# Kernel tuning notes

Hardware: AMD Instinct MI355X
Metric: run time of the kernel (lower is better)

## Reference

```python
import jax, jax.numpy as jnp
import numpy as np

B, T, IN = 4096, 512, 1
H, L = 50, 2


def setup_inputs() -> dict:
    key = jax.random.key(0)
    ks = jax.random.split(key, 11)
    s_in = 1.0 / np.sqrt(H)  # PyTorch LSTM init scale
    def u(k, shape):
        return jax.random.uniform(k, shape, jnp.float32, -s_in, s_in)
    return {
        "x": jax.random.normal(ks[0], (B, T, IN), jnp.float32),
        # layer 0 (gate order i, f, g, o stacked along first axis, like torch)
        "W_ih0": u(ks[1], (4 * H, IN)),
        "W_hh0": u(ks[2], (4 * H, H)),
        "b_ih0": u(ks[3], (4 * H,)),
        "b_hh0": u(ks[4], (4 * H,)),
        # layer 1
        "W_ih1": u(ks[5], (4 * H, H)),
        "W_hh1": u(ks[6], (4 * H, H)),
        "b_ih1": u(ks[7], (4 * H,)),
        "b_hh1": u(ks[8], (4 * H,)),
        # final linear projection hidden -> 1
        "fc_w": u(ks[9], (1, H)),
        "fc_b": u(ks[10], (1,)),
    }


def _lstm_layer(x_tbf, W_ih, W_hh, b_ih, b_hh):
    """x_tbf: [T, B, F] -> outputs [T, B, H]. Zero initial (h, c)."""
    # Precompute input contribution for all timesteps at once: [T, B, 4H]
    gates_x = jnp.einsum('tbf,gf->tbg', x_tbf, W_ih) + b_ih + b_hh

    def step(carry, gx):
        h, c = carry
        g = gx + h @ W_hh.T  # [B, 4H]
        i, f, gg, o = jnp.split(g, 4, axis=-1)
        i = jax.nn.sigmoid(i)
        f = jax.nn.sigmoid(f)
        gg = jnp.tanh(gg)
        o = jax.nn.sigmoid(o)
        c = f * c + i * gg
        h = o * jnp.tanh(c)
        return (h, c), h

    Bsz = x_tbf.shape[1]
    h0 = jnp.zeros((Bsz, W_hh.shape[1]), x_tbf.dtype)
    (_, _), hs = jax.lax.scan(step, (h0, h0), gates_x)
    return hs  # [T, B, H]


def reference(x, W_ih0, W_hh0, b_ih0, b_hh0, W_ih1, W_hh1, b_ih1, b_hh1, fc_w, fc_b):
    x_tbf = jnp.transpose(x, (1, 0, 2))  # [T, B, IN]
    h1 = _lstm_layer(x_tbf, W_ih0, W_hh0, b_ih0, b_hh0)   # [T, B, H]
    h2 = _lstm_layer(h1, W_ih1, W_hh1, b_ih1, b_hh1)      # [T, B, H]
    last = h2[-1]                                         # [B, H] == out[:, -1, :]
    return last @ fc_w.T + fc_b                           # [B, 1]
```

## Files before the change

### kernel.cpp

```cpp
#include <hip/hip_runtime.h>


typedef _Float16 half8 __attribute__((ext_vector_type(8)));
typedef float    f32x4 __attribute__((ext_vector_type(4)));

#define TT   512
#define HID  50
#define NB   16

__device__ __forceinline__ float sigm(float v) {
    return __builtin_amdgcn_rcpf(1.0f + __expf(-v));
}
__device__ __forceinline__ float tanhh(float v) {
    return 1.0f - 2.0f * __builtin_amdgcn_rcpf(1.0f + __expf(2.0f * v));
}

__device__ __forceinline__ float4 make_wfrag(const float* W, const float* Wx,
                                             int gate, int cell, int chunk,
                                             int quad, bool foldx) {
    half8 hv = {};
    #pragma unroll
    for (int j = 0; j < 8; ++j) {
        const int k = 32 * chunk + 8 * quad + j;
        float v = 0.0f;
        if (cell < HID) {
            if (k < HID)                 v = W[(gate * HID + cell) * HID + k];
            else if (foldx && k == HID)  v = Wx[gate * HID + cell];
        }
        hv[j] = (_Float16)v;
    }
    return __builtin_bit_cast(float4, hv);
}

#define PIN(f) asm volatile("" : "+v"(f.x), "+v"(f.y), "+v"(f.z), "+v"(f.w));
#define MFMA(af, b, c) __builtin_amdgcn_mfma_f32_16x16x32_f16(__builtin_bit_cast(half8, (af)), (b), (c), 0, 0, 0)

extern "C" __global__ __launch_bounds__(832, 4)
void lstm2_mfma_kernel(const float* __restrict__ x,
                       const float* __restrict__ W_ih0, const float* __restrict__ W_hh0,
                       const float* __restrict__ b_ih0, const float* __restrict__ b_hh0,
                       const float* __restrict__ W_ih1, const float* __restrict__ W_hh1,
                       const float* __restrict__ b_ih1, const float* __restrict__ b_hh1,
                       const float* __restrict__ fc_w, const float* __restrict__ fc_b,
                       float* __restrict__ out)
{
    __shared__ _Float16 H0[2][1024];
    __shared__ _Float16 H1[2][1024];
    __shared__ float    hfin[HID * NB];

    const int tid  = threadIdx.x;
    const int lane = tid & 63;
    const int wv   = tid >> 6;
    const int b0   = blockIdx.x * NB;

    for (int i = tid; i < 1024; i += 832) {
        H0[0][i] = (_Float16)0.f; H0[1][i] = (_Float16)0.f;
        H1[0][i] = (_Float16)0.f; H1[1][i] = (_Float16)0.f;
    }

    const int quad = lane >> 4;
    const int col  = lane & 15;

    const int mrow  = lane & 15;
    const int gateA = mrow & 3;
    const int cellA = 4 * wv + (mrow >> 2);
    float4 A0c0 = make_wfrag(W_hh0, W_ih0, gateA, cellA, 0, quad, true);
    float4 A0c1 = make_wfrag(W_hh0, W_ih0, gateA, cellA, 1, quad, true);
    float4 Aic0 = make_wfrag(W_ih1, W_ih1, gateA, cellA, 0, quad, false);
    float4 Aic1 = make_wfrag(W_ih1, W_ih1, gateA, cellA, 1, quad, false);
    float4 Ahc0 = make_wfrag(W_hh1, W_hh1, gateA, cellA, 0, quad, false);
    float4 Ahc1 = make_wfrag(W_hh1, W_hh1, gateA, cellA, 1, quad, false);
    PIN(A0c0) PIN(A0c1) PIN(Aic0) PIN(Aic1) PIN(Ahc0) PIN(Ahc1)

    const int  cellD = 4 * wv + quad;
    const bool ewok  = (cellD < HID);
    f32x4 bias0, bias1;
    #pragma unroll
    for (int g = 0; g < 4; ++g) {
        bias0[g] = ewok ? b_ih0[g * HID + cellD] + b_hh0[g * HID + cellD] : 0.f;
        bias1[g] = ewok ? b_ih1[g * HID + cellD] + b_hh1[g * HID + cellD] : 0.f;
    }
    const int wi = (cellD >> 5) * 512 + (((cellD & 31) >> 3) * 16 + col) * 8 + (cellD & 7);

    if (tid < NB) H0[0][512 + (32 + tid) * 8 + 2] = (_Float16)x[(size_t)(b0 + tid) * TT];

    float c0 = 0.f, c1 = 0.f;
    __syncthreads();

    #pragma unroll 2
    for (int u = 0; u <= TT; ++u) {
        const int pu = u & 1, pn = pu ^ 1;

        half8 b0c0 = *(half8*)(&H0[pu][lane * 8]);
        half8 b0c1 = *(half8*)(&H0[pu][512 + lane * 8]);

        float xr = 0.f;
        if (tid < NB && (u + 1) < TT)
            xr = x[(size_t)(b0 + tid) * TT + u + 1];

        if (u != TT) {
            f32x4 acc = bias0;
            acc = MFMA(A0c0, b0c0, acc);
            acc = MFMA(A0c1, b0c1, acc);
            c0 = sigm(acc[1]) * c0 + sigm(acc[0]) * tanhh(acc[2]);
            const float h = sigm(acc[3]) * tanhh(c0);
            if (ewok) H0[pn][wi] = (_Float16)h;
        }
        if (u != 0) {
            half8 b1c0 = *(half8*)(&H1[pn][lane * 8]);
            half8 b1c1 = *(half8*)(&H1[pn][512 + lane * 8]);
            f32x4 acc = bias1;
            acc = MFMA(Aic0, b0c0, acc);
            acc = MFMA(Aic1, b0c1, acc);
            acc = MFMA(Ahc0, b1c0, acc);
            acc = MFMA(Ahc1, b1c1, acc);
            c1 = sigm(acc[1]) * c1 + sigm(acc[0]) * tanhh(acc[2]);
            const float h = sigm(acc[3]) * tanhh(c1);
            if (ewok) {
                H1[pu][wi] = (_Float16)h;
                if (u == TT) hfin[cellD * NB + col] = h;
            }
        }
        if (tid < NB && (u + 1) < TT)
            H0[pn][512 + (32 + tid) * 8 + 2] = (_Float16)xr;
        __syncthreads();
    }

    if (tid < NB) {
        float s = fc_b[0];
        for (int k = 0; k < HID; ++k)
            s += fc_w[k] * hfin[k * NB + tid];
        out[b0 + tid] = s;
    }
}

extern "C" void kernel_launch(void* const* d_in, const int* in_sizes, int n_in,
                              void* d_out, int out_size, void* d_ws, size_t ws_size,
                              hipStream_t stream) {
    (void)in_sizes; (void)n_in; (void)d_ws; (void)ws_size; (void)out_size;
    const float* x     = (const float*)d_in[0];
    const float* W_ih0 = (const float*)d_in[1];
    const float* W_hh0 = (const float*)d_in[2];
    const float* b_ih0 = (const float*)d_in[3];
    const float* b_hh0 = (const float*)d_in[4];
    const float* W_ih1 = (const float*)d_in[5];
    const float* W_hh1 = (const float*)d_in[6];
    const float* b_ih1 = (const float*)d_in[7];
    const float* b_hh1 = (const float*)d_in[8];
    const float* fc_w  = (const float*)d_in[9];
    const float* fc_b  = (const float*)d_in[10];

    dim3 grid(4096 / NB);
    dim3 block(832);
    lstm2_mfma_kernel<<<grid, block, 0, stream>>>(
        x, W_ih0, W_hh0, b_ih0, b_hh0,
        W_ih1, W_hh1, b_ih1, b_hh1,
        fc_w, fc_b, (float*)d_out);
}
```

Before: 471.4 us.

## Prescale gate weights by log2e, fuse activations, stage x in LDS

```diff
diff --git a/kernel.cpp b/kernel.cpp
--- a/kernel.cpp
+++ b/kernel.cpp
@@ -7,29 +7,33 @@
 #define TT   512
 #define HID  50
 #define NB   16
+#define LOG2E 1.44269504f
 
-__device__ __forceinline__ float sigm(float v) {
-    return __builtin_amdgcn_rcpf(1.0f + __expf(-v));
-}
-__device__ __forceinline__ float tanhh(float v) {
-    return 1.0f - 2.0f * __builtin_amdgcn_rcpf(1.0f + __expf(2.0f * v));
-}
-
-__device__ __forceinline__ float4 make_wfrag(const float* W, const float* Wx,
-                                             int gate, int cell, int chunk,
-                                             int quad, bool foldx) {
+__device__ __forceinline__ float4 make_wfrag(const float* W, int gate, int cell,
+                                             int chunk, int quad, float scale) {
     half8 hv = {};
     #pragma unroll
     for (int j = 0; j < 8; ++j) {
         const int k = 32 * chunk + 8 * quad + j;
         float v = 0.0f;
-        if (cell < HID) {
-            if (k < HID)                 v = W[(gate * HID + cell) * HID + k];
-            else if (foldx && k == HID)  v = Wx[gate * HID + cell];
-        }
+        if (cell < HID && k < HID) v = W[(gate * HID + cell) * HID + k] * scale;
         hv[j] = (_Float16)v;
     }
     return __builtin_bit_cast(float4, hv);
+}
+
+__device__ __forceinline__ float cell_update(const f32x4 a, float& c) {
+    const float ei = __builtin_exp2f(a[0]);
+    const float ef = __builtin_exp2f(a[1]);
+    const float eg = __builtin_exp2f(a[2]);
+    const float eo = __builtin_exp2f(a[3]);
+    const float itg = (eg - 1.0f) *
+        __builtin_amdgcn_rcpf((1.0f + ei) * (eg + 1.0f));
+    const float sf = __builtin_amdgcn_rcpf(1.0f + ef);
+    c = sf * c + itg;
+    const float ec = __builtin_exp2f(c * (2.0f * LOG2E));
+    return (ec - 1.0f) *
+        __builtin_amdgcn_rcpf((1.0f + eo) * (ec + 1.0f));
 }
 
 #define PIN(f) asm volatile("" : "+v"(f.x), "+v"(f.y), "+v"(f.z), "+v"(f.w));
@@ -46,6 +50,7 @@
 {
     __shared__ _Float16 H0[2][1024];
     __shared__ _Float16 H1[2][1024];
+    __shared__ float    xs[NB * TT];
     __shared__ float    hfin[HID * NB];
 
     const int tid  = threadIdx.x;
@@ -57,6 +62,11 @@
         H0[0][i] = (_Float16)0.f; H0[1][i] = (_Float16)0.f;
         H1[0][i] = (_Float16)0.f; H1[1][i] = (_Float16)0.f;
     }
+    {
+        const float4* src = (const float4*)(x + (size_t)b0 * TT);
+        float4* dst = (float4*)xs;
+        for (int i = tid; i < NB * TT / 4; i += 832) dst[i] = src[i];
+    }
 
     const int quad = lane >> 4;
     const int col  = lane & 15;
@@ -64,25 +74,27 @@
     const int mrow  = lane & 15;
     const int gateA = mrow & 3;
     const int cellA = 4 * wv + (mrow >> 2);
-    float4 A0c0 = make_wfrag(W_hh0, W_ih0, gateA, cellA, 0, quad, true);
-    float4 A0c1 = make_wfrag(W_hh0, W_ih0, gateA, cellA, 1, quad, true);
-    float4 Aic0 = make_wfrag(W_ih1, W_ih1, gateA, cellA, 0, quad, false);
-    float4 Aic1 = make_wfrag(W_ih1, W_ih1, gateA, cellA, 1, quad, false);
-    float4 Ahc0 = make_wfrag(W_hh1, W_hh1, gateA, cellA, 0, quad, false);
-    float4 Ahc1 = make_wfrag(W_hh1, W_hh1, gateA, cellA, 1, quad, false);
+    const float scA = (gateA == 2) ? 2.0f * LOG2E : -LOG2E;
+    float4 A0c0 = make_wfrag(W_hh0, gateA, cellA, 0, quad, scA);
+    float4 A0c1 = make_wfrag(W_hh0, gateA, cellA, 1, quad, scA);
+    float4 Aic0 = make_wfrag(W_ih1, gateA, cellA, 0, quad, scA);
+    float4 Aic1 = make_wfrag(W_ih1, gateA, cellA, 1, quad, scA);
+    float4 Ahc0 = make_wfrag(W_hh1, gateA, cellA, 0, quad, scA);
+    float4 Ahc1 = make_wfrag(W_hh1, gateA, cellA, 1, quad, scA);
     PIN(A0c0) PIN(A0c1) PIN(Aic0) PIN(Aic1) PIN(Ahc0) PIN(Ahc1)
 
     const int  cellD = 4 * wv + quad;
     const bool ewok  = (cellD < HID);
-    f32x4 bias0, bias1;
+    f32x4 bias0, bias1, wx0;
     #pragma unroll
     for (int g = 0; g < 4; ++g) {
-        bias0[g] = ewok ? b_ih0[g * HID + cellD] + b_hh0[g * HID + cellD] : 0.f;
-        bias1[g] = ewok ? b_ih1[g * HID + cellD] + b_hh1[g * HID + cellD] : 0.f;
+        const float s = (g == 2) ? 2.0f * LOG2E : -LOG2E;
+        bias0[g] = ewok ? (b_ih0[g * HID + cellD] + b_hh0[g * HID + cellD]) * s : 0.f;
+        bias1[g] = ewok ? (b_ih1[g * HID + cellD] + b_hh1[g * HID + cellD]) * s : 0.f;
+        wx0[g]   = ewok ? W_ih0[g * HID + cellD] * s : 0.f;
     }
+    PIN(wx0)
     const int wi = (cellD >> 5) * 512 + (((cellD & 31) >> 3) * 16 + col) * 8 + (cellD & 7);
-
-    if (tid < NB) H0[0][512 + (32 + tid) * 8 + 2] = (_Float16)x[(size_t)(b0 + tid) * TT];
 
     float c0 = 0.f, c1 = 0.f;
     __syncthreads();
@@ -94,16 +106,14 @@
         half8 b0c0 = *(half8*)(&H0[pu][lane * 8]);
         half8 b0c1 = *(half8*)(&H0[pu][512 + lane * 8]);
 
-        float xr = 0.f;
-        if (tid < NB && (u + 1) < TT)
-            xr = x[(size_t)(b0 + tid) * TT + u + 1];
-
         if (u != TT) {
+            const float xv = xs[col * TT + u];
             f32x4 acc = bias0;
+            #pragma unroll
+            for (int g = 0; g < 4; ++g) acc[g] += wx0[g] * xv;
             acc = MFMA(A0c0, b0c0, acc);
             acc = MFMA(A0c1, b0c1, acc);
-            c0 = sigm(acc[1]) * c0 + sigm(acc[0]) * tanhh(acc[2]);
-            const float h = sigm(acc[3]) * tanhh(c0);
+            const float h = cell_update(acc, c0);
             if (ewok) H0[pn][wi] = (_Float16)h;
         }
         if (u != 0) {
@@ -114,15 +124,12 @@
             acc = MFMA(Aic1, b0c1, acc);
             acc = MFMA(Ahc0, b1c0, acc);
             acc = MFMA(Ahc1, b1c1, acc);
-            c1 = sigm(acc[1]) * c1 + sigm(acc[0]) * tanhh(acc[2]);
-            const float h = sigm(acc[3]) * tanhh(c1);
+            const float h = cell_update(acc, c1);
             if (ewok) {
                 H1[pu][wi] = (_Float16)h;
                 if (u == TT) hfin[cellD * NB + col] = h;
             }
         }
-        if (tid < NB && (u + 1) < TT)
-            H0[pn][512 + (32 + tid) * 8 + 2] = (_Float16)xr;
         __syncthreads();
     }
 
```

After: 627.6 us. 1.33x slower.
